# Performance work log

Measured on AMD Instinct MI355X. Metric: run time of the kernel, lower is better.

Reference implementation:

```python
import jax, jax.numpy as jnp
import numpy as np

B = 8192
DIMS = [5, 1024, 1024, 512, 512, 512, 512, 2]  # model_param
L1, L2, OBS_X, OBS_Y, R = 3.0, 3.0, 0.0, 7.0, 4.0


def _linear_params(key, fan_in, fan_out):
    kw, kb = jax.random.split(key)
    lim = 1.0 / np.sqrt(fan_in)
    W = jax.random.uniform(kw, (fan_in, fan_out), jnp.float32, -lim, lim)
    b = jax.random.uniform(kb, (fan_out,), jnp.float32, -lim, lim)
    return W, b


def setup_inputs() -> dict:
    key = jax.random.key(0)
    keys = jax.random.split(key, 9)
    x = jax.random.normal(keys[0], (B, DIMS[0]), jnp.float32)
    W1, b1 = _linear_params(keys[1], DIMS[0], DIMS[1])
    W2, b2 = _linear_params(keys[2], DIMS[1], DIMS[2])
    W31, b31 = _linear_params(keys[3], DIMS[2], DIMS[3])
    W32, b32 = _linear_params(keys[4], DIMS[2], DIMS[4])
    W41, b41 = _linear_params(keys[5], DIMS[3], DIMS[5])
    W42, b42 = _linear_params(keys[6], DIMS[4], DIMS[6])
    W51, b51 = _linear_params(keys[7], DIMS[5], DIMS[7])
    W52, b52 = _linear_params(keys[8], DIMS[6], DIMS[7])
    return {
        'x': x, 'sgn': 1,
        'mean': jnp.zeros((DIMS[0],), jnp.float32),
        'std': jnp.ones((DIMS[0],), jnp.float32),
        'mean_label': jnp.zeros((2,), jnp.float32),
        'std_label': jnp.ones((2,), jnp.float32),
        'W1': W1, 'b1': b1, 'W2': W2, 'b2': b2,
        'W31': W31, 'b31': b31, 'W32': W32, 'b32': b32,
        'W41': W41, 'b41': b41, 'W42': W42, 'b42': b42,
        'W51': W51, 'b51': b51, 'W52': W52, 'b52': b52,
    }


def _forward(x, mean, std, mean_label, std_label,
             W1, b1, W2, b2, W31, b31, W32, b32,
             W41, b41, W42, b42, W51, b51, W52, b52):
    act = jax.nn.relu
    x0 = x * std + mean                      # un-normalized state [B,5]
    x1 = act(x @ W1 + b1)
    x2 = act(x1 @ W2 + b2)
    x31 = act(x2 @ W31 + b31)
    x32 = act(x2 @ W32 + b32)
    x41 = act(x31 @ W41 + b41)
    x42 = act(x32 @ W42 + b42)
    x51 = x41 @ W51 + b51                    # QP linear term p  [B,2]
    x52 = 4.0 * jax.nn.sigmoid(x42 @ W52 + b52)  # CBF class-K gains [B,2]

    # dCBF terms (two-link arm obstacle barrier)
    t1, w1, t2, w2 = x0[:, 0], x0[:, 1], x0[:, 2], x0[:, 3]
    s1, s2, c1, c2 = jnp.sin(t1), jnp.sin(t2), jnp.cos(t1), jnp.cos(t2)
    px = L1 * c1 + L2 * c2 - OBS_X
    py = L1 * s1 + L2 * s2 - OBS_Y
    vx = -L1 * s1 * w1 - L2 * s2 * w2
    vy = L1 * c1 * w1 + L2 * c2 * w2
    barrier = px * px + py * py - R * R
    b_dot = 2.0 * (px * vx + py * vy)
    Lf2b = (2.0 * (vx * vx + vy * vy)
            + 2.0 * px * (-L1 * c1 * w1 * w1 - L2 * c2 * w2 * w2)
            + 2.0 * py * (-L1 * s1 * w1 * w1 - L2 * s2 * w2 * w2))
    # G (single inequality row, 2 columns), G u <= h
    G1 = -(2.0 * px * (-L1 * s1) + 2.0 * py * (L1 * c1))
    G2 = -(2.0 * px * (-L2 * s2) + 2.0 * py * (L2 * c2))
    G = jnp.stack([G1, G2], axis=1)          # [B,2]
    h = Lf2b + (x52[:, 0] + x52[:, 1]) * b_dot + x52[:, 0] * x52[:, 1] * barrier  # [B]

    # QP: min 0.5||u||^2 + x51.u  s.t. G u <= h  -> closed-form KKT projection
    u0 = -x51                                 # unconstrained optimum
    viol = jnp.sum(G * u0, axis=1) - h        # [B]
    lam = jnp.maximum(viol, 0.0) / (jnp.sum(G * G, axis=1) + 1e-12)
    u = u0 - lam[:, None] * G                 # [B,2]
    return (u - mean_label) / std_label


def reference(x, sgn, mean, std, mean_label, std_label,
              W1, b1, W2, b2, W31, b31, W32, b32,
              W41, b41, W42, b42, W51, b51, W52, b52):
    # sgn == 1 -> batched QP branch (the trained/deployed path)
    return _forward(x, mean, std, mean_label, std_label,
                    W1, b1, W2, b2, W31, b31, W32, b32,
                    W41, b41, W42, b42, W51, b51, W52, b52)
```

## Files before the change

kernel.cpp:

```cpp
#include <hip/hip_runtime.h>
#include <hip/hip_bf16.h>
#include <math.h>


typedef __attribute__((ext_vector_type(4))) float f32x4;
typedef __attribute__((ext_vector_type(8))) short bf16x8;

static __device__ __forceinline__ unsigned short f2bf(float f) {
    unsigned int u = __float_as_uint(f);
    unsigned int r = (u + 0x7fffu + ((u >> 16) & 1u)) >> 16;
    return (unsigned short)r;
}
static __device__ __forceinline__ float bf2f(unsigned short h) {
    return __uint_as_float(((unsigned int)h) << 16);
}

#define TBM 128
#define TBN 256
#define TBK 64

#define GLL(gp, lp) __builtin_amdgcn_global_load_lds( \
    (const __attribute__((address_space(1))) void*)(gp), \
    (__attribute__((address_space(3))) void*)(lp), 16, 0, 0)

#define LGKM0() asm volatile("s_waitcnt lgkmcnt(0)" ::: "memory")
#define VMC(N)  asm volatile("s_waitcnt vmcnt(" #N ")" ::: "memory")
#define BAR()   __builtin_amdgcn_s_barrier()
#define SB0()   __builtin_amdgcn_sched_barrier(0)

__device__ __forceinline__ void gemm_core(
    const unsigned short* __restrict__ A, int lda,
    const unsigned short* __restrict__ Bt, int ldb,
    const float* __restrict__ bias,
    unsigned short* __restrict__ C, int ldc,
    int K, int m0, int n0b, int c0)
{
    __shared__ __align__(16) short sA0[TBM * TBK], sA1[TBM * TBK];
    __shared__ __align__(16) short sB0v[TBN * TBK], sB1v[TBN * TBK];

    const int tid  = threadIdx.x;
    const int w    = tid >> 6;
    const int lane = tid & 63;

    const int srow = lane >> 3;
    const int skq  = (lane & 7) ^ ((lane >> 3) & 7);
    const unsigned short* aP0 =
        A + (size_t)(m0 + 16 * w + srow) * lda + skq * 8;
    const unsigned short* aP1 = aP0 + 8 * lda;
    const unsigned short* bP0 =
        Bt + (size_t)(n0b + 32 * w + srow) * ldb + skq * 8;
    const unsigned short* bP1 = bP0 + 8 * ldb;
    const unsigned short* bP2 = bP0 + 16 * ldb;
    const unsigned short* bP3 = bP0 + 24 * ldb;

    const int wrow = (w >> 2) * 64;
    const int wcol = (w & 3) * 64;
    const int fr = lane & 15;
    const int fq = lane >> 4;
    const int swz0 = ((fq)     ^ (fr & 7)) * 8;
    const int swz1 = ((4 + fq) ^ (fr & 7)) * 8;

    f32x4 acc[4][4] = {};
    const int nt = K / TBK;

    auto STAGE = [&](int kt, short* la, short* lb) {
        const size_t ko = (size_t)kt * TBK;
        GLL(aP0 + ko, la + (2 * w)     * 512);
        GLL(aP1 + ko, la + (2 * w + 1) * 512);
        GLL(bP0 + ko, lb + (4 * w)     * 512);
        GLL(bP1 + ko, lb + (4 * w + 1) * 512);
        GLL(bP2 + ko, lb + (4 * w + 2) * 512);
        GLL(bP3 + ko, lb + (4 * w + 3) * 512);
    };

    auto BODY = [&](int t, short* sAp, short* sBp) {
        bf16x8 af[2][4], bf[2][4];
        #pragma unroll
        for (int m = 0; m < 4; ++m) {
            const int r = (wrow + m * 16 + fr) * 64;
            af[0][m] = *reinterpret_cast<const bf16x8*>(&sAp[r + swz0]);
            af[1][m] = *reinterpret_cast<const bf16x8*>(&sAp[r + swz1]);
        }
        #pragma unroll
        for (int n = 0; n < 4; ++n) {
            const int r = (wcol + n * 16 + fr) * 64;
            bf[0][n] = *reinterpret_cast<const bf16x8*>(&sBp[r + swz0]);
            bf[1][n] = *reinterpret_cast<const bf16x8*>(&sBp[r + swz1]);
        }
        LGKM0();
        BAR();
        SB0();
        if (t + 2 < nt) STAGE(t + 2, sAp, sBp);
        #pragma unroll
        for (int kh = 0; kh < 2; ++kh)
            #pragma unroll
            for (int m = 0; m < 4; ++m)
                #pragma unroll
                for (int n = 0; n < 4; ++n)
                    acc[m][n] = __builtin_amdgcn_mfma_f32_16x16x32_bf16(
                        af[kh][m], bf[kh][n], acc[m][n], 0, 0, 0);
        if (t + 1 < nt) {
            if (t + 2 < nt) { VMC(6); } else { VMC(0); }
            BAR();
            SB0();
        }
    };

    STAGE(0, sA0, sB0v);
    STAGE(1, sA1, sB1v);
    VMC(6);
    BAR();
    SB0();

    for (int t = 0; t < nt; t += 2) {
        BODY(t,     sA0, sB0v);
        BODY(t + 1, sA1, sB1v);
    }

    #pragma unroll
    for (int n = 0; n < 4; ++n) {
        const int cl = wcol + n * 16 + fr;
        const float bv = bias[n0b + cl];
        #pragma unroll
        for (int m = 0; m < 4; ++m) {
            const int rbase = m0 + wrow + m * 16 + fq * 4;
            #pragma unroll
            for (int r = 0; r < 4; ++r) {
                float v = fmaxf(acc[m][n][r] + bv, 0.0f);
                C[(size_t)(rbase + r) * ldc + c0 + cl] = f2bf(v);
            }
        }
    }
}

__global__ __launch_bounds__(512, 2) void gemm_bf16(
    const unsigned short* __restrict__ A, int lda,
    const unsigned short* __restrict__ Bt, int ldb,
    const float* __restrict__ bias,
    unsigned short* __restrict__ C, int ldc, int K)
{
    const int n0 = blockIdx.x * TBN;
    const int m0 = blockIdx.y * TBM;
    gemm_core(A, lda, Bt, ldb, bias, C, ldc, K, m0, n0, n0);
}

__global__ __launch_bounds__(512, 2) void gemm_bf16_l4(
    const unsigned short* __restrict__ x3,
    const unsigned short* __restrict__ W41t,
    const unsigned short* __restrict__ W42t,
    const float* __restrict__ b41, const float* __restrict__ b42,
    unsigned short* __restrict__ x4)
{
    const int g   = blockIdx.x >> 1;
    const int n0b = (blockIdx.x & 1) * TBN;
    const int m0  = blockIdx.y * TBM;
    const unsigned short* A  = x3 + (g ? 512 : 0);
    const unsigned short* Bt = g ? W42t : W41t;
    const float* bias        = g ? b42 : b41;
    gemm_core(A, 1024, Bt, 512, bias, x4, 1024, 512, m0, n0b, g * 512 + n0b);
}

__global__ __launch_bounds__(256) void prep_weights(
    const float* __restrict__ W2,  const float* __restrict__ W31,
    const float* __restrict__ W32, const float* __restrict__ W41,
    const float* __restrict__ W42, const float* __restrict__ b31,
    const float* __restrict__ b32,
    unsigned short* __restrict__ W2t,  unsigned short* __restrict__ W3t,
    unsigned short* __restrict__ W41t, unsigned short* __restrict__ W42t,
    float* __restrict__ b3c)
{
    const int z = blockIdx.z;
    if (z == 5) {
        if (blockIdx.x == 0 && blockIdx.y == 0) {
            for (int i = threadIdx.x; i < 1024; i += 256)
                b3c[i] = (i < 512) ? b31[i] : b32[i - 512];
        }
        return;
    }
    const float* src; unsigned short* dst; int K, N;
    switch (z) {
        case 0:  src = W2;  dst = W2t;              K = 1024; N = 1024; break;
        case 1:  src = W31; dst = W3t;              K = 1024; N = 512;  break;
        case 2:  src = W32; dst = W3t + 512 * 1024; K = 1024; N = 512;  break;
        case 3:  src = W41; dst = W41t;             K = 512;  N = 512;  break;
        default: src = W42; dst = W42t;             K = 512;  N = 512;  break;
    }
    const int k0 = blockIdx.x * 32, n0 = blockIdx.y * 32;
    if (k0 >= K || n0 >= N) return;

    __shared__ float t[32][33];
    const int tx = threadIdx.x & 31, ty = threadIdx.x >> 5;
    #pragma unroll
    for (int i = 0; i < 32; i += 8)
        t[ty + i][tx] = src[(size_t)(k0 + ty + i) * N + n0 + tx];
    __syncthreads();
    #pragma unroll
    for (int i = 0; i < 32; i += 8)
        dst[(size_t)(n0 + ty + i) * K + k0 + tx] = f2bf(t[tx][ty + i]);
}

__global__ __launch_bounds__(256) void layer1_kernel(
    const float* __restrict__ x, const float* __restrict__ W1,
    const float* __restrict__ b1, unsigned short* __restrict__ x1out)
{
    const int row = blockIdx.x;
    const int j4 = threadIdx.x * 4;
    float xr[5];
    #pragma unroll
    for (int k = 0; k < 5; ++k) xr[k] = x[row * 5 + k];
    float4 acc = *reinterpret_cast<const float4*>(&b1[j4]);
    #pragma unroll
    for (int k = 0; k < 5; ++k) {
        float4 wv = *reinterpret_cast<const float4*>(&W1[k * 1024 + j4]);
        acc.x = fmaf(xr[k], wv.x, acc.x);
        acc.y = fmaf(xr[k], wv.y, acc.y);
        acc.z = fmaf(xr[k], wv.z, acc.z);
        acc.w = fmaf(xr[k], wv.w, acc.w);
    }
    ushort4 o;
    o.x = f2bf(fmaxf(acc.x, 0.f));
    o.y = f2bf(fmaxf(acc.y, 0.f));
    o.z = f2bf(fmaxf(acc.z, 0.f));
    o.w = f2bf(fmaxf(acc.w, 0.f));
    *reinterpret_cast<ushort4*>(&x1out[(size_t)row * 1024 + j4]) = o;
}

__global__ __launch_bounds__(256) void head_kernel(
    const unsigned short* __restrict__ x4,
    const float* __restrict__ W51, const float* __restrict__ b51,
    const float* __restrict__ W52, const float* __restrict__ b52,
    const float* __restrict__ x,   const float* __restrict__ mean,
    const float* __restrict__ stdv, const float* __restrict__ mean_label,
    const float* __restrict__ std_label, float* __restrict__ out)
{
    const int wave = threadIdx.x >> 6;
    const int lane = threadIdx.x & 63;
    const int row = blockIdx.x * 4 + wave;

    const unsigned short* p41 = x4 + (size_t)row * 1024;
    const unsigned short* p42 = p41 + 512;

    float a0 = 0.f, a1 = 0.f, a2 = 0.f, a3 = 0.f;
    #pragma unroll
    for (int it = 0; it < 8; ++it) {
        const int k = lane + it * 64;
        const float v1 = bf2f(p41[k]);
        const float2 w5 = *reinterpret_cast<const float2*>(&W51[k * 2]);
        a0 = fmaf(v1, w5.x, a0);
        a1 = fmaf(v1, w5.y, a1);
        const float v2 = bf2f(p42[k]);
        const float2 w6 = *reinterpret_cast<const float2*>(&W52[k * 2]);
        a2 = fmaf(v2, w6.x, a2);
        a3 = fmaf(v2, w6.y, a3);
    }
    #pragma unroll
    for (int off = 32; off >= 1; off >>= 1) {
        a0 += __shfl_down(a0, off);
        a1 += __shfl_down(a1, off);
        a2 += __shfl_down(a2, off);
        a3 += __shfl_down(a3, off);
    }

    if (lane == 0) {
        const float L1c = 3.0f, L2c = 3.0f, OBSX = 0.0f, OBSY = 7.0f, Rc = 4.0f;
        const float t1 = x[row * 5 + 0] * stdv[0] + mean[0];
        const float w1 = x[row * 5 + 1] * stdv[1] + mean[1];
        const float t2 = x[row * 5 + 2] * stdv[2] + mean[2];
        const float w2 = x[row * 5 + 3] * stdv[3] + mean[3];
        const float s1 = sinf(t1), c1 = cosf(t1);
        const float s2 = sinf(t2), c2 = cosf(t2);
        const float px = L1c * c1 + L2c * c2 - OBSX;
        const float py = L1c * s1 + L2c * s2 - OBSY;
        const float vx = -L1c * s1 * w1 - L2c * s2 * w2;
        const float vy =  L1c * c1 * w1 + L2c * c2 * w2;
        const float barrier = px * px + py * py - Rc * Rc;
        const float b_dot = 2.0f * (px * vx + py * vy);
        const float Lf2b = 2.0f * (vx * vx + vy * vy)
                         + 2.0f * px * (-L1c * c1 * w1 * w1 - L2c * c2 * w2 * w2)
                         + 2.0f * py * (-L1c * s1 * w1 * w1 - L2c * s2 * w2 * w2);
        const float G1 = -(2.0f * px * (-L1c * s1) + 2.0f * py * (L1c * c1));
        const float G2 = -(2.0f * px * (-L2c * s2) + 2.0f * py * (L2c * c2));

        const float x51_0 = a0 + b51[0];
        const float x51_1 = a1 + b51[1];
        const float z0 = a2 + b52[0];
        const float z1 = a3 + b52[1];
        const float x52_0 = 4.0f / (1.0f + expf(-z0));
        const float x52_1 = 4.0f / (1.0f + expf(-z1));

        const float u0_0 = -x51_0;
        const float u0_1 = -x51_1;
        const float h = Lf2b + (x52_0 + x52_1) * b_dot + x52_0 * x52_1 * barrier;
        const float viol = G1 * u0_0 + G2 * u0_1 - h;
        const float lam = fmaxf(viol, 0.0f) / (G1 * G1 + G2 * G2 + 1e-12f);
        const float u_0 = u0_0 - lam * G1;
        const float u_1 = u0_1 - lam * G2;
        out[row * 2 + 0] = (u_0 - mean_label[0]) / std_label[0];
        out[row * 2 + 1] = (u_1 - mean_label[1]) / std_label[1];
    }
}

extern "C" void kernel_launch(void* const* d_in, const int* in_sizes, int n_in,
                              void* d_out, int out_size, void* d_ws, size_t ws_size,
                              hipStream_t stream) {
    const float* x          = (const float*)d_in[0];
    const float* mean       = (const float*)d_in[2];
    const float* stdv       = (const float*)d_in[3];
    const float* mean_label = (const float*)d_in[4];
    const float* std_label  = (const float*)d_in[5];
    const float* W1  = (const float*)d_in[6];   const float* b1  = (const float*)d_in[7];
    const float* W2  = (const float*)d_in[8];   const float* b2  = (const float*)d_in[9];
    const float* W31 = (const float*)d_in[10];  const float* b31 = (const float*)d_in[11];
    const float* W32 = (const float*)d_in[12];  const float* b32 = (const float*)d_in[13];
    const float* W41 = (const float*)d_in[14];  const float* b41 = (const float*)d_in[15];
    const float* W42 = (const float*)d_in[16];  const float* b42 = (const float*)d_in[17];
    const float* W51 = (const float*)d_in[18];  const float* b51 = (const float*)d_in[19];
    const float* W52 = (const float*)d_in[20];  const float* b52 = (const float*)d_in[21];
    float* out = (float*)d_out;

    char* ws = (char*)d_ws;
    const size_t MiB = 1024 * 1024;
    unsigned short* xb1  = (unsigned short*)(ws + 0);
    unsigned short* x2b  = (unsigned short*)(ws + 16 * MiB);
    unsigned short* x3   = xb1;
    unsigned short* x4   = x2b;
    unsigned short* W2t  = (unsigned short*)(ws + 32 * MiB);
    unsigned short* W3t  = (unsigned short*)(ws + 34 * MiB);
    unsigned short* W41t = (unsigned short*)(ws + 36 * MiB);
    unsigned short* W42t = (unsigned short*)(ws + 36 * MiB + 512 * 1024);
    float*          b3c  = (float*)(ws + 37 * MiB);

    prep_weights<<<dim3(32, 32, 6), 256, 0, stream>>>(
        W2, W31, W32, W41, W42, b31, b32, W2t, W3t, W41t, W42t, b3c);

    layer1_kernel<<<8192, 256, 0, stream>>>(x, W1, b1, xb1);

    dim3 gBig(1024 / TBN, 8192 / TBM);
    gemm_bf16<<<gBig, 512, 0, stream>>>(xb1, 1024, W2t, 1024, b2, x2b, 1024, 1024);
    gemm_bf16<<<gBig, 512, 0, stream>>>(x2b, 1024, W3t, 1024, b3c, x3, 1024, 1024);

    gemm_bf16_l4<<<dim3(4, 64), 512, 0, stream>>>(x3, W41t, W42t, b41, b42, x4);

    head_kernel<<<2048, 256, 0, stream>>>(x4, W51, b51, W52, b52,
                                          x, mean, stdv, mean_label, std_label, out);
}
```

Measured before the change: 88.86 us.

## Triple-buffer GEMM pipeline, XCD-aware block remap, fuse layer1 into prep, vectorize head

The GEMM main loop moves from two LDS buffers to three. This drops one barrier and the lgkmcnt wait per k-step, and the MFMA block is wrapped in s_setprio. Blocks are remapped so neighbouring tiles land on the same XCD for L2 reuse, and the layer-1 kernel is folded into prep_weights as an extra grid slice, saving one launch. The head kernel now uses 16-byte vector loads per lane instead of strided scalar loads. The larger LDS footprint (144KB per block) may limit the 2-blocks-per-CU occupancy, and removing the LDS-read wait before the barrier needs care about hazards.

```diff
diff --git a/kernel.cpp b/kernel.cpp
--- a/kernel.cpp
+++ b/kernel.cpp
@@ -23,7 +23,6 @@
     (const __attribute__((address_space(1))) void*)(gp), \
     (__attribute__((address_space(3))) void*)(lp), 16, 0, 0)
 
-#define LGKM0() asm volatile("s_waitcnt lgkmcnt(0)" ::: "memory")
 #define VMC(N)  asm volatile("s_waitcnt vmcnt(" #N ")" ::: "memory")
 #define BAR()   __builtin_amdgcn_s_barrier()
 #define SB0()   __builtin_amdgcn_sched_barrier(0)
@@ -35,8 +34,8 @@
     unsigned short* __restrict__ C, int ldc,
     int K, int m0, int n0b, int c0)
 {
-    __shared__ __align__(16) short sA0[TBM * TBK], sA1[TBM * TBK];
-    __shared__ __align__(16) short sB0v[TBN * TBK], sB1v[TBN * TBK];
+    __shared__ __align__(16) short sA[3][TBM * TBK];
+    __shared__ __align__(16) short sB[3][TBN * TBK];
 
     const int tid  = threadIdx.x;
     const int w    = tid >> 6;
@@ -63,8 +62,10 @@
     f32x4 acc[4][4] = {};
     const int nt = K / TBK;
 
-    auto STAGE = [&](int kt, short* la, short* lb) {
+    auto STAGE = [&](int kt, int b) {
         const size_t ko = (size_t)kt * TBK;
+        short* la = &sA[b][0];
+        short* lb = &sB[b][0];
         GLL(aP0 + ko, la + (2 * w)     * 512);
         GLL(aP1 + ko, la + (2 * w + 1) * 512);
         GLL(bP0 + ko, lb + (4 * w)     * 512);
@@ -73,7 +74,17 @@
         GLL(bP3 + ko, lb + (4 * w + 3) * 512);
     };
 
-    auto BODY = [&](int t, short* sAp, short* sBp) {
+    STAGE(0, 0);
+    STAGE(1, 1);
+    VMC(6);
+    BAR();
+    SB0();
+
+    int cur = 0, stg = 2;
+    for (int t = 0; t < nt; ++t) {
+        const short* sAp = &sA[cur][0];
+        const short* sBp = &sB[cur][0];
+
         bf16x8 af[2][4], bf[2][4];
         #pragma unroll
         for (int m = 0; m < 4; ++m) {
@@ -87,10 +98,10 @@
             bf[0][n] = *reinterpret_cast<const bf16x8*>(&sBp[r + swz0]);
             bf[1][n] = *reinterpret_cast<const bf16x8*>(&sBp[r + swz1]);
         }
-        LGKM0();
-        BAR();
-        SB0();
-        if (t + 2 < nt) STAGE(t + 2, sAp, sBp);
+
+        if (t + 2 < nt) STAGE(t + 2, stg);
+
+        __builtin_amdgcn_s_setprio(1);
         #pragma unroll
         for (int kh = 0; kh < 2; ++kh)
             #pragma unroll
@@ -99,22 +110,15 @@
                 for (int n = 0; n < 4; ++n)
                     acc[m][n] = __builtin_amdgcn_mfma_f32_16x16x32_bf16(
                         af[kh][m], bf[kh][n], acc[m][n], 0, 0, 0);
+        __builtin_amdgcn_s_setprio(0);
+
         if (t + 1 < nt) {
             if (t + 2 < nt) { VMC(6); } else { VMC(0); }
             BAR();
             SB0();
         }
-    };
-
-    STAGE(0, sA0, sB0v);
-    STAGE(1, sA1, sB1v);
-    VMC(6);
-    BAR();
-    SB0();
-
-    for (int t = 0; t < nt; t += 2) {
-        BODY(t,     sA0, sB0v);
-        BODY(t + 1, sA1, sB1v);
+        cur = (cur == 2) ? 0 : cur + 1;
+        stg = (stg == 2) ? 0 : stg + 1;
     }
 
     #pragma unroll
@@ -133,14 +137,20 @@
     }
 }
 
+static __device__ __forceinline__ int xcd_sid() {
+    const int bid = blockIdx.y * gridDim.x + blockIdx.x;
+    return (bid & 7) * 32 + (bid >> 3);
+}
+
 __global__ __launch_bounds__(512, 2) void gemm_bf16(
     const unsigned short* __restrict__ A, int lda,
     const unsigned short* __restrict__ Bt, int ldb,
     const float* __restrict__ bias,
     unsigned short* __restrict__ C, int ldc, int K)
 {
-    const int n0 = blockIdx.x * TBN;
-    const int m0 = blockIdx.y * TBM;
+    const int sid = xcd_sid();
+    const int n0 = (sid & 3) * TBN;
+    const int m0 = (sid >> 2) * TBM;
     gemm_core(A, lda, Bt, ldb, bias, C, ldc, K, m0, n0, n0);
 }
 
@@ -151,9 +161,11 @@
     const float* __restrict__ b41, const float* __restrict__ b42,
     unsigned short* __restrict__ x4)
 {
-    const int g   = blockIdx.x >> 1;
-    const int n0b = (blockIdx.x & 1) * TBN;
-    const int m0  = blockIdx.y * TBM;
+    const int sid = xcd_sid();
+    const int xp  = sid & 3;
+    const int g   = xp >> 1;
+    const int n0b = (xp & 1) * TBN;
+    const int m0  = (sid >> 2) * TBM;
     const unsigned short* A  = x3 + (g ? 512 : 0);
     const unsigned short* Bt = g ? W42t : W41t;
     const float* bias        = g ? b42 : b41;
@@ -165,11 +177,42 @@
     const float* __restrict__ W32, const float* __restrict__ W41,
     const float* __restrict__ W42, const float* __restrict__ b31,
     const float* __restrict__ b32,
+    const float* __restrict__ x,   const float* __restrict__ W1,
+    const float* __restrict__ b1,
     unsigned short* __restrict__ W2t,  unsigned short* __restrict__ W3t,
     unsigned short* __restrict__ W41t, unsigned short* __restrict__ W42t,
-    float* __restrict__ b3c)
+    float* __restrict__ b3c, unsigned short* __restrict__ xb1)
 {
     const int z = blockIdx.z;
+    if (z == 6) {
+        const int r0 = (blockIdx.y * 32 + blockIdx.x) * 8;
+        const int j4 = threadIdx.x * 4;
+        float4 wv[5];
+        #pragma unroll
+        for (int k = 0; k < 5; ++k)
+            wv[k] = *reinterpret_cast<const float4*>(&W1[k * 1024 + j4]);
+        const float4 bb = *reinterpret_cast<const float4*>(&b1[j4]);
+        #pragma unroll
+        for (int r = 0; r < 8; ++r) {
+            const float* xr = &x[(size_t)(r0 + r) * 5];
+            float4 acc = bb;
+            #pragma unroll
+            for (int k = 0; k < 5; ++k) {
+                const float xv = xr[k];
+                acc.x = fmaf(xv, wv[k].x, acc.x);
+                acc.y = fmaf(xv, wv[k].y, acc.y);
+                acc.z = fmaf(xv, wv[k].z, acc.z);
+                acc.w = fmaf(xv, wv[k].w, acc.w);
+            }
+            ushort4 o;
+            o.x = f2bf(fmaxf(acc.x, 0.f));
+            o.y = f2bf(fmaxf(acc.y, 0.f));
+            o.z = f2bf(fmaxf(acc.z, 0.f));
+            o.w = f2bf(fmaxf(acc.w, 0.f));
+            *reinterpret_cast<ushort4*>(&xb1[(size_t)(r0 + r) * 1024 + j4]) = o;
+        }
+        return;
+    }
     if (z == 5) {
         if (blockIdx.x == 0 && blockIdx.y == 0) {
             for (int i = threadIdx.x; i < 1024; i += 256)
@@ -199,32 +242,6 @@
         dst[(size_t)(n0 + ty + i) * K + k0 + tx] = f2bf(t[tx][ty + i]);
 }
 
-__global__ __launch_bounds__(256) void layer1_kernel(
-    const float* __restrict__ x, const float* __restrict__ W1,
-    const float* __restrict__ b1, unsigned short* __restrict__ x1out)
-{
-    const int row = blockIdx.x;
-    const int j4 = threadIdx.x * 4;
-    float xr[5];
-    #pragma unroll
-    for (int k = 0; k < 5; ++k) xr[k] = x[row * 5 + k];
-    float4 acc = *reinterpret_cast<const float4*>(&b1[j4]);
-    #pragma unroll
-    for (int k = 0; k < 5; ++k) {
-        float4 wv = *reinterpret_cast<const float4*>(&W1[k * 1024 + j4]);
-        acc.x = fmaf(xr[k], wv.x, acc.x);
-        acc.y = fmaf(xr[k], wv.y, acc.y);
-        acc.z = fmaf(xr[k], wv.z, acc.z);
-        acc.w = fmaf(xr[k], wv.w, acc.w);
-    }
-    ushort4 o;
-    o.x = f2bf(fmaxf(acc.x, 0.f));
-    o.y = f2bf(fmaxf(acc.y, 0.f));
-    o.z = f2bf(fmaxf(acc.z, 0.f));
-    o.w = f2bf(fmaxf(acc.w, 0.f));
-    *reinterpret_cast<ushort4*>(&x1out[(size_t)row * 1024 + j4]) = o;
-}
-
 __global__ __launch_bounds__(256) void head_kernel(
     const unsigned short* __restrict__ x4,
     const float* __restrict__ W51, const float* __restrict__ b51,
@@ -238,20 +255,31 @@
     const int row = blockIdx.x * 4 + wave;
 
     const unsigned short* p41 = x4 + (size_t)row * 1024;
-    const unsigned short* p42 = p41 + 512;
-
-    float a0 = 0.f, a1 = 0.f, a2 = 0.f, a3 = 0.f;
-    #pragma unroll
-    for (int it = 0; it < 8; ++it) {
-        const int k = lane + it * 64;
-        const float v1 = bf2f(p41[k]);
-        const float2 w5 = *reinterpret_cast<const float2*>(&W51[k * 2]);
-        a0 = fmaf(v1, w5.x, a0);
-        a1 = fmaf(v1, w5.y, a1);
-        const float v2 = bf2f(p42[k]);
-        const float2 w6 = *reinterpret_cast<const float2*>(&W52[k * 2]);
-        a2 = fmaf(v2, w6.x, a2);
-        a3 = fmaf(v2, w6.y, a3);
+    const bf16x8 v1 = *reinterpret_cast<const bf16x8*>(p41 + lane * 8);
+    const bf16x8 v2 = *reinterpret_cast<const bf16x8*>(p41 + 512 + lane * 8);
+    const float4 q0 = *reinterpret_cast<const float4*>(W51 + lane * 16 + 0);
+    const float4 q1 = *reinterpret_cast<const float4*>(W51 + lane * 16 + 4);
+    const float4 q2 = *reinterpret_cast<const float4*>(W51 + lane * 16 + 8);
+    const float4 q3 = *reinterpret_cast<const float4*>(W51 + lane * 16 + 12);
+    const float4 s0 = *reinterpret_cast<const float4*>(W52 + lane * 16 + 0);
+    const float4 s1 = *reinterpret_cast<const float4*>(W52 + lane * 16 + 4);
+    const float4 s2 = *reinterpret_cast<const float4*>(W52 + lane * 16 + 8);
+    const float4 s3 = *reinterpret_cast<const float4*>(W52 + lane * 16 + 12);
+
+    float a0, a1, a2, a3;
+    {
+        const float e0 = bf2f((unsigned short)v1[0]), e1 = bf2f((unsigned short)v1[1]),
+                    e2 = bf2f((unsigned short)v1[2]), e3 = bf2f((unsigned short)v1[3]),
+                    e4 = bf2f((unsigned short)v1[4]), e5 = bf2f((unsigned short)v1[5]),
+                    e6 = bf2f((unsigned short)v1[6]), e7 = bf2f((unsigned short)v1[7]);
+        a0 = e0*q0.x + e1*q0.z + e2*q1.x + e3*q1.z + e4*q2.x + e5*q2.z + e6*q3.x + e7*q3.z;
+        a1 = e0*q0.y + e1*q0.w + e2*q1.y + e3*q1.w + e4*q2.y + e5*q2.w + e6*q3.y + e7*q3.w;
+        const float f0 = bf2f((unsigned short)v2[0]), f1 = bf2f((unsigned short)v2[1]),
+                    f2 = bf2f((unsigned short)v2[2]), f3 = bf2f((unsigned short)v2[3]),
+                    f4 = bf2f((unsigned short)v2[4]), f5 = bf2f((unsigned short)v2[5]),
+                    f6 = bf2f((unsigned short)v2[6]), f7 = bf2f((unsigned short)v2[7]);
+        a2 = f0*s0.x + f1*s0.z + f2*s1.x + f3*s1.z + f4*s2.x + f5*s2.z + f6*s3.x + f7*s3.z;
+        a3 = f0*s0.y + f1*s0.w + f2*s1.y + f3*s1.w + f4*s2.y + f5*s2.w + f6*s3.y + f7*s3.w;
     }
     #pragma unroll
     for (int off = 32; off >= 1; off >>= 1) {
@@ -267,19 +295,19 @@
         const float w1 = x[row * 5 + 1] * stdv[1] + mean[1];
         const float t2 = x[row * 5 + 2] * stdv[2] + mean[2];
         const float w2 = x[row * 5 + 3] * stdv[3] + mean[3];
-        const float s1 = sinf(t1), c1 = cosf(t1);
-        const float s2 = sinf(t2), c2 = cosf(t2);
+        const float s1v = sinf(t1), c1 = cosf(t1);
+        const float s2v = sinf(t2), c2 = cosf(t2);
         const float px = L1c * c1 + L2c * c2 - OBSX;
-        const float py = L1c * s1 + L2c * s2 - OBSY;
-        const float vx = -L1c * s1 * w1 - L2c * s2 * w2;
+        const float py = L1c * s1v + L2c * s2v - OBSY;
+        const float vx = -L1c * s1v * w1 - L2c * s2v * w2;
         const float vy =  L1c * c1 * w1 + L2c * c2 * w2;
         const float barrier = px * px + py * py - Rc * Rc;
         const float b_dot = 2.0f * (px * vx + py * vy);
         const float Lf2b = 2.0f * (vx * vx + vy * vy)
                          + 2.0f * px * (-L1c * c1 * w1 * w1 - L2c * c2 * w2 * w2)
-                         + 2.0f * py * (-L1c * s1 * w1 * w1 - L2c * s2 * w2 * w2);
-        const float G1 = -(2.0f * px * (-L1c * s1) + 2.0f * py * (L1c * c1));
-        const float G2 = -(2.0f * px * (-L2c * s2) + 2.0f * py * (L2c * c2));
+                         + 2.0f * py * (-L1c * s1v * w1 * w1 - L2c * s2v * w2 * w2);
+        const float G1 = -(2.0f * px * (-L1c * s1v) + 2.0f * py * (L1c * c1));
+        const float G2 = -(2.0f * px * (-L2c * s2v) + 2.0f * py * (L2c * c2));
 
         const float x51_0 = a0 + b51[0];
         const float x51_1 = a1 + b51[1];
@@ -330,10 +358,9 @@
     unsigned short* W42t = (unsigned short*)(ws + 36 * MiB + 512 * 1024);
     float*          b3c  = (float*)(ws + 37 * MiB);
 
-    prep_weights<<<dim3(32, 32, 6), 256, 0, stream>>>(
-        W2, W31, W32, W41, W42, b31, b32, W2t, W3t, W41t, W42t, b3c);
-
-    layer1_kernel<<<8192, 256, 0, stream>>>(x, W1, b1, xb1);
+    prep_weights<<<dim3(32, 32, 7), 256, 0, stream>>>(
+        W2, W31, W32, W41, W42, b31, b32, x, W1, b1,
+        W2t, W3t, W41t, W42t, b3c, xb1);
 
     dim3 gBig(1024 / TBN, 8192 / TBM);
     gemm_bf16<<<gBig, 512, 0, stream>>>(xb1, 1024, W2t, 1024, b2, x2b, 1024, 1024);
```

Measured after the change: 78.95 us, median of 2. 1.13x faster.
